# Kernel tuning notes

Measured on AMD Instinct MI355X. Metric: run time of the kernel, lower is better.

The kernel has to match this reference:

```python
import jax, jax.numpy as jnp
import numpy as np

U = 2048
D = 2048
N_HEADS = 16
D_HEAD = D // N_HEADS
FFN_MULT = 4
D_FF = FFN_MULT * D
EPS = 1e-6


def _rmsnorm(x, w):
    # x: [U, D], w: [D]
    ms = jnp.mean(jnp.square(x), axis=-1, keepdims=True)
    return x * jax.lax.rsqrt(ms + EPS) * w


def setup_inputs() -> dict:
    key = jax.random.key(0)
    ks = jax.random.split(key, 12)
    d = {}
    d["x"] = jax.random.normal(ks[0], (U, D), dtype=jnp.float32)
    d["adj_bias"] = jax.random.normal(ks[1], (U, U), dtype=jnp.float32)
    # learned params (torch nn.Linear stores weight as [out, in]; y = x @ W.T)
    init = lambda k, shape, std: jax.random.normal(k, shape, dtype=jnp.float32) * std
    d["norm1_w"] = jnp.ones((D,), dtype=jnp.float32)
    d["norm2_w"] = jnp.ones((D,), dtype=jnp.float32)
    d["wq"] = init(ks[2], (D, D), (1.0 / D) ** 0.5)
    d["wk"] = init(ks[3], (D, D), (1.0 / D) ** 0.5)
    d["wv"] = init(ks[4], (D, D), (1.0 / D) ** 0.5)
    d["wo"] = init(ks[5], (D, D), (2.0 / D) ** 0.5)  # nn.init.normal_ std=(2/D)^0.5
    d["w_up"] = init(ks[6], (D_FF, D), (1.0 / D) ** 0.5)
    d["b_up"] = jnp.zeros((D_FF,), dtype=jnp.float32)
    d["w_down"] = init(ks[7], (D, D_FF), (2.0 / D_FF) ** 0.5)
    d["b_down"] = jnp.zeros((D,), dtype=jnp.float32)
    return d


def reference(x, adj_bias, norm1_w, norm2_w, wq, wk, wv, wo, w_up, b_up, w_down, b_down):
    scale = 1.0 / (D_HEAD ** 0.5)
    h = _rmsnorm(x, norm1_w)
    # project and split heads: [U, D] -> [H, U, d]
    q = (h @ wq.T).reshape(U, N_HEADS, D_HEAD).transpose(1, 0, 2)
    k = (h @ wk.T).reshape(U, N_HEADS, D_HEAD).transpose(1, 0, 2)
    v = (h @ wv.T).reshape(U, N_HEADS, D_HEAD).transpose(1, 0, 2)
    scores = jnp.einsum('hud,hvd->huv', q, k) * scale + adj_bias[None, :, :]
    attn = jax.nn.softmax(scores, axis=-1)
    out = jnp.einsum('huv,hvd->hud', attn, v)  # [H, U, d]
    out = out.transpose(1, 0, 2).reshape(U, D)
    x = x + out @ wo.T
    h2 = _rmsnorm(x, norm2_w)
    ff = jax.nn.gelu(h2 @ w_up.T + b_up, approximate=False)
    x = x + ff @ w_down.T + b_down
    return x
```

## Files before the change

### kernel.cpp

```cpp
#include <hip/hip_runtime.h>
#include <hip/hip_fp16.h>
#include <cstdint>
#include <cstddef>

#define U_DIM 2048
#define D_DIM 2048
#define NH 16
#define DH 128
#define DFF 8192
#define EPS_RMS 1e-6f
#define ATTN_SCALE 0.088388347648318447f

typedef unsigned short u16;
typedef __attribute__((ext_vector_type(4))) float floatx4;
typedef __attribute__((ext_vector_type(8))) short shortx8;

__device__ __forceinline__ float bf2f(u16 u) {
  union { unsigned int i; float f; } v; v.i = ((unsigned int)u) << 16; return v.f;
}
__device__ __forceinline__ u16 f2bf(float f) {
  union { float f; unsigned int i; } v; v.f = f;
  return (u16)((v.i + 0x7fffu + ((v.i >> 16) & 1u)) >> 16);
}
__device__ __forceinline__ u16 f2h(float f) {
  __half h = __float2half_rn(f);
  union { __half h; u16 u; } c; c.h = h; return c.u;
}
__device__ __forceinline__ float h2f(u16 u) {
  union { __half h; u16 u; } c; c.u = u; return __half2float(c.h);
}

__global__ __launch_bounds__(256) void k_f2b(const float* __restrict__ in,
                                             u16* __restrict__ out, int n4) {
  int i = blockIdx.x * 256 + threadIdx.x;
  if (i >= n4) return;
  float4 f = reinterpret_cast<const float4*>(in)[i];
  ushort4 o;
  o.x = f2bf(f.x); o.y = f2bf(f.y); o.z = f2bf(f.z); o.w = f2bf(f.w);
  reinterpret_cast<ushort4*>(out)[i] = o;
}

__global__ __launch_bounds__(256) void k_prep_bias(const float* __restrict__ adj,
                                                   u16* __restrict__ adjp) {
  const int tile = blockIdx.x;
  const int qt = tile >> 4, kt = tile & 15;
  const int t = threadIdx.x;
  const int c16 = t & 15, rblk = t >> 4;
  u16* outt = adjp + (size_t)tile * 16384;
#pragma unroll
  for (int rr = 0; rr < 8; rr++) {
    int r = rblk * 8 + rr;
    const float* src = adj + (size_t)(qt * 128 + r) * U_DIM + kt * 128 + c16;
    ushort4 o0, o1;
    o0.x = f2h(src[0]);    o0.y = f2h(src[16]);  o0.z = f2h(src[32]);  o0.w = f2h(src[48]);
    o1.x = f2h(src[64]);   o1.y = f2h(src[80]);  o1.z = f2h(src[96]);  o1.w = f2h(src[112]);
    ushort4* dst = reinterpret_cast<ushort4*>(outt + ((size_t)c16 * 128 + r) * 8);
    dst[0] = o0; dst[1] = o1;
  }
}

__global__ __launch_bounds__(256) void k_reduce4(
    const u16* __restrict__ p0, const u16* __restrict__ p1,
    const u16* __restrict__ p2, const u16* __restrict__ p3,
    const float* __restrict__ X, const float* __restrict__ bias,
    float* __restrict__ out, int n4) {
  int i = blockIdx.x * 256 + threadIdx.x;
  if (i >= n4) return;
  ushort4 a = reinterpret_cast<const ushort4*>(p0)[i];
  ushort4 b = reinterpret_cast<const ushort4*>(p1)[i];
  ushort4 c = reinterpret_cast<const ushort4*>(p2)[i];
  ushort4 d = reinterpret_cast<const ushort4*>(p3)[i];
  float4 xv = reinterpret_cast<const float4*>(X)[i];
  float4 r;
  r.x = xv.x + bf2f(a.x) + bf2f(b.x) + bf2f(c.x) + bf2f(d.x);
  r.y = xv.y + bf2f(a.y) + bf2f(b.y) + bf2f(c.y) + bf2f(d.y);
  r.z = xv.z + bf2f(a.z) + bf2f(b.z) + bf2f(c.z) + bf2f(d.z);
  r.w = xv.w + bf2f(a.w) + bf2f(b.w) + bf2f(c.w) + bf2f(d.w);
  if (bias) {
    int col = (i * 4) & (D_DIM - 1);
    float4 bv = *reinterpret_cast<const float4*>(bias + col);
    r.x += bv.x; r.y += bv.y; r.z += bv.z; r.w += bv.w;
  }
  reinterpret_cast<float4*>(out)[i] = r;
}

__global__ __launch_bounds__(256) void k_rmsnorm(const float* __restrict__ x,
                                                 const float* __restrict__ w,
                                                 u16* __restrict__ out) {
  const int row = blockIdx.x;
  const int t = threadIdx.x;
  const float4* xr = reinterpret_cast<const float4*>(x + (size_t)row * D_DIM);
  float4 a0 = xr[t], a1 = xr[t + 256];
  float ss = a0.x*a0.x + a0.y*a0.y + a0.z*a0.z + a0.w*a0.w
           + a1.x*a1.x + a1.y*a1.y + a1.z*a1.z + a1.w*a1.w;
#pragma unroll
  for (int off = 32; off > 0; off >>= 1) ss += __shfl_xor(ss, off);
  __shared__ float red[4];
  if ((t & 63) == 0) red[t >> 6] = ss;
  __syncthreads();
  float tot = red[0] + red[1] + red[2] + red[3];
  float r = rsqrtf(tot / (float)D_DIM + EPS_RMS);
  const float4* wr = reinterpret_cast<const float4*>(w);
  float4 w0 = wr[t], w1 = wr[t + 256];
  ushort4 o0, o1;
  o0.x = f2bf(a0.x * r * w0.x); o0.y = f2bf(a0.y * r * w0.y);
  o0.z = f2bf(a0.z * r * w0.z); o0.w = f2bf(a0.w * r * w0.w);
  o1.x = f2bf(a1.x * r * w1.x); o1.y = f2bf(a1.y * r * w1.y);
  o1.z = f2bf(a1.z * r * w1.z); o1.w = f2bf(a1.w * r * w1.w);
  ushort4* op = reinterpret_cast<ushort4*>(out + (size_t)row * D_DIM);
  op[t] = o0; op[t + 256] = o1;
}

__device__ __forceinline__ void async16(u16* lds, const u16* g) {
  __builtin_amdgcn_global_load_lds(
      (__attribute__((address_space(1))) void*)(g),
      (__attribute__((address_space(3))) void*)(lds), 16, 0, 0);
}

#define BK64 64

__device__ __forceinline__ void gemm256_core(
    const u16* __restrict__ A, int lda,
    const u16* __restrict__ B, int ldb,
    int K, int bm, int bn, u16* smem, floatx4 acc[8][4]) {
  const int t = threadIdx.x;
  const int wv = t >> 6, lane = t & 63;
  const int wm = wv >> 2, wn = wv & 3;
  const int fr = lane & 15, kq = lane >> 4;
  const int srow = wv * 8 + (lane >> 3);
  const int scg  = (lane & 7) ^ (lane >> 3);
  const u16* Ag = A + (size_t)(bm + srow) * lda + scg * 8;
  const u16* Bg = B + (size_t)(bn + srow) * ldb + scg * 8;
  u16* AsW = smem + (wv * 8) * 64;
  u16* BsW = smem + 32768 + (wv * 8) * 64;
  const int swz  = fr & 7;
  const int arow = wm * 128 + fr;
  const int brow = wn * 64 + fr;
  const int nt = K / BK64;
#pragma unroll
  for (int r = 0; r < 4; r++) async16(AsW + r * 4096, Ag + (size_t)(r * 64) * lda);
#pragma unroll
  for (int r = 0; r < 4; r++) async16(BsW + r * 4096, Bg + (size_t)(r * 64) * ldb);
  int cur = 0;
  for (int kt = 0; kt < nt; kt++) {
    asm volatile("s_waitcnt vmcnt(0)" ::: "memory");
    __builtin_amdgcn_sched_barrier(0);
    __builtin_amdgcn_s_barrier();
    asm volatile("" ::: "memory");
    if (kt + 1 < nt) {
      const int nb = (cur ^ 1) * 16384;
      const size_t ko = (size_t)(kt + 1) * BK64;
#pragma unroll
      for (int r = 0; r < 4; r++) async16(AsW + nb + r * 4096, Ag + (size_t)(r * 64) * lda + ko);
#pragma unroll
      for (int r = 0; r < 4; r++) async16(BsW + nb + r * 4096, Bg + (size_t)(r * 64) * ldb + ko);
    }
    const u16* Ab = smem + cur * 16384;
    const u16* Bb = smem + 32768 + cur * 16384;
    shortx8 af[4], bf[4];
#pragma unroll
    for (int ph = 0; ph < 4; ph++) {
      const int ksub = ph >> 1;
      const int mh   = ph & 1;
      const int cswz = (((ksub * 4 + kq) ^ swz) * 8);
      if (mh == 0) {
#pragma unroll
        for (int i = 0; i < 4; i++)
          af[i] = *reinterpret_cast<const shortx8*>(Ab + (arow + i * 16) * 64 + cswz);
#pragma unroll
        for (int i = 0; i < 4; i++)
          bf[i] = *reinterpret_cast<const shortx8*>(Bb + (brow + i * 16) * 64 + cswz);
      } else {
#pragma unroll
        for (int i = 0; i < 4; i++)
          af[i] = *reinterpret_cast<const shortx8*>(Ab + (arow + (i + 4) * 16) * 64 + cswz);
      }
      asm volatile("s_waitcnt lgkmcnt(0)" ::: "memory");
      __builtin_amdgcn_sched_barrier(0);
      __builtin_amdgcn_s_setprio(1);
      const int m0 = mh * 4;
#pragma unroll
      for (int i = 0; i < 4; i++)
#pragma unroll
        for (int j = 0; j < 4; j++)
          acc[m0 + i][j] = __builtin_amdgcn_mfma_f32_16x16x32_bf16(af[i], bf[j], acc[m0 + i][j], 0, 0, 0);
      __builtin_amdgcn_s_setprio(0);
      if (ph < 3) { __builtin_amdgcn_s_barrier(); asm volatile("" ::: "memory"); }
    }
    cur ^= 1;
  }
}

#define GEMM256_PRELUDE                                           \
  __shared__ u16 smem[65536];                         \
  floatx4 acc[8][4];                                              \
  {                                                               \
    floatx4 zf = {0.f, 0.f, 0.f, 0.f};                            \
    for (int i = 0; i < 8; i++)                                   \
      for (int j = 0; j < 4; j++) acc[i][j] = zf;                 \
  }                                                               \
  const int bm = blockIdx.y * 256, bn = blockIdx.x * 256;

#define EPILOG256                                                 \
  const int lane_ = threadIdx.x & 63;                             \
  const int wv_ = threadIdx.x >> 6;                               \
  const int fr_ = lane_ & 15, kq_ = lane_ >> 4;                   \
  const int row0 = (wv_ >> 2) * 128 + kq_ * 4;                    \
  const int col0 = (wv_ & 3) * 64 + fr_;

__global__ __launch_bounds__(512, 1) void k_gemm_qkv(
    const u16* __restrict__ A, const u16* __restrict__ B,
    u16* __restrict__ Q, u16* __restrict__ Ko, u16* __restrict__ VT) {
  GEMM256_PRELUDE;
  gemm256_core(A, D_DIM, B, D_DIM, D_DIM, bm, bn, smem, acc);
  EPILOG256;
  if (bn < 4096) {
    u16* C = (bn < 2048) ? Q : Ko;
    const int cb = (bn < 2048) ? bn : bn - 2048;
#pragma unroll
    for (int mt = 0; mt < 8; mt++)
#pragma unroll
      for (int i = 0; i < 4; i++) {
        u16* cr = C + (size_t)(bm + row0 + mt*16 + i) * D_DIM + cb + col0;
#pragma unroll
        for (int nt = 0; nt < 4; nt++) cr[nt*16] = f2bf(acc[mt][nt][i]);
      }
  } else {
    const int cb = bn - 4096;
#pragma unroll
    for (int mt = 0; mt < 8; mt++)
#pragma unroll
      for (int nt = 0; nt < 4; nt++) {
        int col = cb + col0 + nt*16;
        int row = bm + row0 + mt*16;
        ushort4 o;
        o.x = f2bf(acc[mt][nt][0]); o.y = f2bf(acc[mt][nt][1]);
        o.z = f2bf(acc[mt][nt][2]); o.w = f2bf(acc[mt][nt][3]);
        *reinterpret_cast<ushort4*>(VT + (size_t)col * U_DIM + row) = o;
      }
  }
}

__global__ __launch_bounds__(512, 1) void k_gemm_splitk_part(
    const u16* __restrict__ A, int lda, const u16* __restrict__ B, int ldb,
    int Kc, u16* __restrict__ P, size_t pstride, int ldc) {
  GEMM256_PRELUDE;
  const int koff = blockIdx.z * Kc;
  gemm256_core(A + koff, lda, B + koff, ldb, Kc, bm, bn, smem, acc);
  u16* Pz = P + (size_t)blockIdx.z * pstride;
  EPILOG256;
#pragma unroll
  for (int mt = 0; mt < 8; mt++)
#pragma unroll
    for (int i = 0; i < 4; i++) {
      u16* cr = Pz + (size_t)(bm + row0 + mt*16 + i) * ldc + bn + col0;
#pragma unroll
      for (int nt = 0; nt < 4; nt++) cr[nt*16] = f2bf(acc[mt][nt][i]);
    }
}

__device__ __forceinline__ float fast_gelu(float v) {
  float u = v * (0.79788456080286536f + 0.035677408136300125f * v * v);
  float tt = fminf(fmaxf(2.f * u, -40.f), 40.f);
  float e = __expf(tt);
  return 0.5f * v * (1.f + (e - 1.f) / (e + 1.f));
}

__global__ __launch_bounds__(512, 1) void k_gemm_gelu(
    const u16* __restrict__ A, int lda, const u16* __restrict__ B, int ldb,
    int K, const float* __restrict__ bias, u16* __restrict__ C, int ldc) {
  GEMM256_PRELUDE;
  gemm256_core(A, lda, B, ldb, K, bm, bn, smem, acc);
  EPILOG256;
#pragma unroll
  for (int mt = 0; mt < 8; mt++)
#pragma unroll
    for (int i = 0; i < 4; i++) {
      size_t off = (size_t)(bm + row0 + mt*16 + i) * ldc + bn + col0;
#pragma unroll
      for (int nt = 0; nt < 4; nt++) {
        float v = acc[mt][nt][i] + bias[bn + col0 + nt*16];
        C[off + nt*16] = f2bf(fast_gelu(v));
      }
    }
}

__global__ __launch_bounds__(256) void k_flash(
    const u16* __restrict__ Q, const u16* __restrict__ K,
    const u16* __restrict__ VT, const u16* __restrict__ ADJP,
    u16* __restrict__ O) {
  __shared__ u16 smem[18432];
  const int qt = blockIdx.x, gh = blockIdx.y;
  const int t = threadIdx.x, wv = t >> 6, lane = t & 63;
  const int fr = lane & 15, kq = lane >> 4;
  const int c4 = lane & 3, r4 = lane >> 2;

  const u16* gq = Q + (size_t)(qt * 64) * D_DIM + gh * DH;
  const u16* gk = K + gh * DH;
  const u16* gv = VT + (size_t)(gh * DH) * U_DIM;

#pragma unroll
  for (int it = 0; it < 4; it++) {
    int row = wv * 16 + it * 4 + kq;
    int cg = (fr + row) & 15;
    async16(smem + row * 128 + fr * 8, gq + (size_t)row * D_DIM + cg * 8);
  }
  __builtin_amdgcn_s_waitcnt(0);
  __syncthreads();
  shortx8 qf[4];
#pragma unroll
  for (int ks = 0; ks < 4; ks++) {
    int row = wv * 16 + fr;
    int slot = ((ks * 4 + kq) - row) & 15;
    qf[ks] = *reinterpret_cast<const shortx8*>(smem + row * 128 + slot * 8);
  }
  __syncthreads();

  floatx4 oacc[8];
  float lrow[4];
#pragma unroll
  for (int nt = 0; nt < 8; nt++) { floatx4 z = {0.f,0.f,0.f,0.f}; oacc[nt] = z; }
#pragma unroll
  for (int i = 0; i < 4; i++) lrow[i] = 0.f;

  {
    u16* Ks = smem; u16* Vs = smem + 8192;
#pragma unroll
    for (int it = 0; it < 2; it++) {
      int row = wv * 8 + it * 4 + kq;
      int cg = (fr + row) & 15;
      async16(Ks + row * 128 + fr * 8, gk + (size_t)row * D_DIM + cg * 8);
    }
#pragma unroll
    for (int it = 0; it < 2; it++) {
      int row = wv * 32 + it * 16 + r4;
      int cg = (c4 + (row >> 1)) & 3;
      async16(Vs + row * 32 + c4 * 8, gv + (size_t)row * U_DIM + cg * 8);
    }
  }

  u16* Pb = smem + 16384;
  for (int kt = 0; kt < 64; kt++) {
    const int cur = kt & 1;
    u16* Ks = smem + cur * 4096;
    u16* Vs = smem + 8192 + cur * 4096;
    asm volatile("s_waitcnt vmcnt(0)" ::: "memory");
    __builtin_amdgcn_s_barrier();
    asm volatile("" ::: "memory");
    if (kt < 63) {
      u16* Kn = smem + (1 - cur) * 4096;
      u16* Vn = smem + 8192 + (1 - cur) * 4096;
      const u16* gkn = gk + (size_t)((kt + 1) * 32) * D_DIM;
      const u16* gvn = gv + (kt + 1) * 32;
#pragma unroll
      for (int it = 0; it < 2; it++) {
        int row = wv * 8 + it * 4 + kq;
        int cg = (fr + row) & 15;
        async16(Kn + row * 128 + fr * 8, gkn + (size_t)row * D_DIM + cg * 8);
      }
#pragma unroll
      for (int it = 0; it < 2; it++) {
        int row = wv * 32 + it * 16 + r4;
        int cg = (c4 + (row >> 1)) & 3;
        async16(Vn + row * 32 + c4 * 8, gvn + (size_t)row * U_DIM + cg * 8);
      }
    }

    floatx4 sacc[2];
    { floatx4 z = {0.f,0.f,0.f,0.f}; sacc[0] = z; sacc[1] = z; }
#pragma unroll
    for (int ks = 0; ks < 4; ks++) {
      int slot0 = ((ks * 4 + kq) - fr) & 15;
      shortx8 kf0 = *reinterpret_cast<const shortx8*>(Ks + fr * 128 + slot0 * 8);
      int slot1 = ((ks * 4 + kq) - (16 + fr)) & 15;
      shortx8 kf1 = *reinterpret_cast<const shortx8*>(Ks + (16 + fr) * 128 + slot1 * 8);
      sacc[0] = __builtin_amdgcn_mfma_f32_16x16x32_bf16(qf[ks], kf0, sacc[0], 0, 0, 0);
      sacc[1] = __builtin_amdgcn_mfma_f32_16x16x32_bf16(qf[ks], kf1, sacc[1], 0, 0, 0);
    }

    const u16* bt = ADJP + ((size_t)(qt >> 1) * 16 + (kt >> 2)) * 16384 + (kt & 3) * 2;
#pragma unroll
    for (int i = 0; i < 4; i++) {
      int rl = wv * 16 + kq * 4 + i;
      int r128 = (qt & 1) * 64 + rl;
      ushort2 bh = *reinterpret_cast<const ushort2*>(bt + ((size_t)fr * 128 + r128) * 8);
      float s0 = sacc[0][i] * ATTN_SCALE + h2f(bh.x);
      float s1 = sacc[1][i] * ATTN_SCALE + h2f(bh.y);
      float p0 = __expf(fminf(s0, 80.f));
      float p1 = __expf(fminf(s1, 80.f));
      int slot0 = ((fr >> 3) - (rl >> 1)) & 3;
      Pb[rl * 32 + slot0 * 8 + (fr & 7)] = f2bf(p0);
      int slot1 = (((16 + fr) >> 3) - (rl >> 1)) & 3;
      Pb[rl * 32 + slot1 * 8 + (fr & 7)] = f2bf(p1);
      lrow[i] += p0 + p1;
    }
    asm volatile("s_waitcnt lgkmcnt(0)" ::: "memory");
    __builtin_amdgcn_s_barrier();
    asm volatile("" ::: "memory");

    shortx8 pf;
    {
      int row = wv * 16 + fr;
      int slot = (kq - (row >> 1)) & 3;
      pf = *reinterpret_cast<const shortx8*>(Pb + row * 32 + slot * 8);
    }
#pragma unroll
    for (int nt = 0; nt < 8; nt++) {
      int row = nt * 16 + fr;
      int slot = (kq - (row >> 1)) & 3;
      shortx8 vf = *reinterpret_cast<const shortx8*>(Vs + row * 32 + slot * 8);
      oacc[nt] = __builtin_amdgcn_mfma_f32_16x16x32_bf16(pf, vf, oacc[nt], 0, 0, 0);
    }
  }

#pragma unroll
  for (int i = 0; i < 4; i++) {
    int rl = wv * 16 + kq * 4 + i;
    float l = lrow[i];
    l += __shfl_xor(l, 1);
    l += __shfl_xor(l, 2);
    l += __shfl_xor(l, 4);
    l += __shfl_xor(l, 8);
    float inv = 1.f / l;
    u16* orow = O + (size_t)(qt * 64 + rl) * D_DIM + gh * DH + fr;
#pragma unroll
    for (int nt = 0; nt < 8; nt++)
      orow[nt * 16] = f2bf(oacc[nt][i] * inv);
  }
}

extern "C" void kernel_launch(void* const* d_in, const int* in_sizes, int n_in,
                              void* d_out, int out_size, void* d_ws, size_t ws_size,
                              hipStream_t stream) {
  (void)in_sizes; (void)n_in; (void)out_size; (void)ws_size;
  const float* x      = (const float*)d_in[0];
  const float* adj    = (const float*)d_in[1];
  const float* n1w    = (const float*)d_in[2];
  const float* n2w    = (const float*)d_in[3];
  const float* wq     = (const float*)d_in[4];
  const float* wk     = (const float*)d_in[5];
  const float* wv     = (const float*)d_in[6];
  const float* wo     = (const float*)d_in[7];
  const float* w_up   = (const float*)d_in[8];
  const float* b_up   = (const float*)d_in[9];
  const float* w_down = (const float*)d_in[10];
  const float* b_down = (const float*)d_in[11];
  float* out = (float*)d_out;
  char* ws = (char*)d_ws;
  const size_t MB = 1u << 20;
  u16* hb   = (u16*)(ws + 0*MB);
  u16* qb   = (u16*)(ws + 8*MB);
  u16* kb   = (u16*)(ws + 16*MB);
  u16* vtb  = (u16*)(ws + 24*MB);
  u16* adjp = (u16*)(ws + 32*MB);
  u16* aob  = (u16*)(ws + 40*MB);
  u16* wob  = (u16*)(ws + 48*MB);
  u16* wqkv = (u16*)(ws + 56*MB);
  u16* opp  = (u16*)(ws + 8*MB);
  u16* h2b  = (u16*)(ws + 0*MB);
  u16* wub  = (u16*)(ws + 8*MB);
  u16* ffb  = (u16*)(ws + 40*MB);
  u16* wdb  = (u16*)(ws + 72*MB);
  u16* dpp  = (u16*)(ws + 8*MB);

  dim3 blk(256);
  dim3 blk512(512);
  const int n4d = (D_DIM * D_DIM) / 4;
  const int n4f = (DFF * D_DIM) / 4;
  const size_t szd = (size_t)D_DIM * D_DIM;

  k_f2b<<<(n4d + 255) / 256, blk, 0, stream>>>(wq, wqkv, n4d);
  k_f2b<<<(n4d + 255) / 256, blk, 0, stream>>>(wk, wqkv + szd, n4d);
  k_f2b<<<(n4d + 255) / 256, blk, 0, stream>>>(wv, wqkv + 2*szd, n4d);
  k_f2b<<<(n4d + 255) / 256, blk, 0, stream>>>(wo, wob, n4d);
  k_prep_bias<<<256, blk, 0, stream>>>(adj, adjp);
  k_rmsnorm<<<U_DIM, blk, 0, stream>>>(x, n1w, hb);

  k_gemm_qkv<<<dim3(24, 8), blk512, 0, stream>>>(hb, wqkv, qb, kb, vtb);

  k_flash<<<dim3(32, 16), blk, 0, stream>>>(qb, kb, vtb, adjp, aob);

  k_gemm_splitk_part<<<dim3(8, 8, 4), blk512, 0, stream>>>(
      aob, D_DIM, wob, D_DIM, D_DIM/4, opp, szd, D_DIM);
  k_reduce4<<<(n4d + 255) / 256, blk, 0, stream>>>(
      opp, opp + szd, opp + 2*szd, opp + 3*szd, x, nullptr, out, n4d);

  k_rmsnorm<<<U_DIM, blk, 0, stream>>>(out, n2w, h2b);
  k_f2b<<<(n4f + 255) / 256, blk, 0, stream>>>(w_up, wub, n4f);
  k_gemm_gelu<<<dim3(32, 8), blk512, 0, stream>>>(h2b, D_DIM, wub, D_DIM, D_DIM,
                                                  b_up, ffb, DFF);
  k_f2b<<<(n4f + 255) / 256, blk, 0, stream>>>(w_down, wdb, n4f);
  k_gemm_splitk_part<<<dim3(8, 8, 4), blk512, 0, stream>>>(
      ffb, DFF, wdb, DFF, DFF/4, dpp, szd, D_DIM);
  k_reduce4<<<(n4d + 255) / 256, blk, 0, stream>>>(
      dpp, dpp + szd, dpp + 2*szd, dpp + 3*szd, out, b_down, out, n4d);
}
```

Before: 581.9 us.

## Batch weight conversions, fuse residual reduce with RMSNorm, widen flash KV tile

Merges the four D×D weight casts into one launch and the w_up/w_down casts into another. Fuses the split-K partial reduce and residual add with the second RMSNorm, so the residual is not written and then read back by a separate norm kernel. The flash-attention KV tile grows from 32 to 64 keys per iteration, halving loop trips and barriers at the cost of doubling shared memory, which may lower occupancy.

```diff
diff --git a/kernel.cpp b/kernel.cpp
--- a/kernel.cpp
+++ b/kernel.cpp
@@ -30,14 +30,36 @@
   union { __half h; u16 u; } c; c.u = u; return __half2float(c.h);
 }
 
-__global__ __launch_bounds__(256) void k_f2b(const float* __restrict__ in,
-                                             u16* __restrict__ out, int n4) {
-  int i = blockIdx.x * 256 + threadIdx.x;
+__device__ __forceinline__ void f2b_body(const float* __restrict__ in,
+                                         u16* __restrict__ out, int i, int n4) {
   if (i >= n4) return;
   float4 f = reinterpret_cast<const float4*>(in)[i];
   ushort4 o;
   o.x = f2bf(f.x); o.y = f2bf(f.y); o.z = f2bf(f.z); o.w = f2bf(f.w);
   reinterpret_cast<ushort4*>(out)[i] = o;
+}
+
+__global__ __launch_bounds__(256) void k_f2b4(
+    const float* __restrict__ s0, const float* __restrict__ s1,
+    const float* __restrict__ s2, const float* __restrict__ s3,
+    u16* __restrict__ d0, u16* __restrict__ d1,
+    u16* __restrict__ d2, u16* __restrict__ d3, int n4) {
+  const float* s; u16* d;
+  switch (blockIdx.y) {
+    case 0: s = s0; d = d0; break;
+    case 1: s = s1; d = d1; break;
+    case 2: s = s2; d = d2; break;
+    default: s = s3; d = d3; break;
+  }
+  f2b_body(s, d, blockIdx.x * 256 + threadIdx.x, n4);
+}
+
+__global__ __launch_bounds__(256) void k_f2b2(
+    const float* __restrict__ s0, const float* __restrict__ s1,
+    u16* __restrict__ d0, u16* __restrict__ d1, int n4) {
+  const float* s = blockIdx.y ? s1 : s0;
+  u16* d = blockIdx.y ? d1 : d0;
+  f2b_body(s, d, blockIdx.x * 256 + threadIdx.x, n4);
 }
 
 __global__ __launch_bounds__(256) void k_prep_bias(const float* __restrict__ adj,
@@ -84,6 +106,51 @@
   reinterpret_cast<float4*>(out)[i] = r;
 }
 
+__global__ __launch_bounds__(256) void k_reduce4norm(
+    const u16* __restrict__ p0, const u16* __restrict__ p1,
+    const u16* __restrict__ p2, const u16* __restrict__ p3,
+    const float* __restrict__ X, const float* __restrict__ w,
+    float* __restrict__ out, u16* __restrict__ nrm) {
+  const int row = blockIdx.x;
+  const int t = threadIdx.x;
+  const size_t base = (size_t)row * 512;
+  float4 r[2];
+  float ss = 0.f;
+#pragma unroll
+  for (int h = 0; h < 2; h++) {
+    size_t i = base + t + h * 256;
+    ushort4 a = reinterpret_cast<const ushort4*>(p0)[i];
+    ushort4 b = reinterpret_cast<const ushort4*>(p1)[i];
+    ushort4 c = reinterpret_cast<const ushort4*>(p2)[i];
+    ushort4 d = reinterpret_cast<const ushort4*>(p3)[i];
+    float4 xv = reinterpret_cast<const float4*>(X)[i];
+    float4 v;
+    v.x = xv.x + bf2f(a.x) + bf2f(b.x) + bf2f(c.x) + bf2f(d.x);
+    v.y = xv.y + bf2f(a.y) + bf2f(b.y) + bf2f(c.y) + bf2f(d.y);
+    v.z = xv.z + bf2f(a.z) + bf2f(b.z) + bf2f(c.z) + bf2f(d.z);
+    v.w = xv.w + bf2f(a.w) + bf2f(b.w) + bf2f(c.w) + bf2f(d.w);
+    reinterpret_cast<float4*>(out)[i] = v;
+    ss += v.x*v.x + v.y*v.y + v.z*v.z + v.w*v.w;
+    r[h] = v;
+  }
+#pragma unroll
+  for (int off = 32; off > 0; off >>= 1) ss += __shfl_xor(ss, off);
+  __shared__ float red[4];
+  if ((t & 63) == 0) red[t >> 6] = ss;
+  __syncthreads();
+  float tot = red[0] + red[1] + red[2] + red[3];
+  float rms = rsqrtf(tot / (float)D_DIM + EPS_RMS);
+  const float4* wr = reinterpret_cast<const float4*>(w);
+#pragma unroll
+  for (int h = 0; h < 2; h++) {
+    float4 wv = wr[t + h * 256];
+    ushort4 o;
+    o.x = f2bf(r[h].x * rms * wv.x); o.y = f2bf(r[h].y * rms * wv.y);
+    o.z = f2bf(r[h].z * rms * wv.z); o.w = f2bf(r[h].w * rms * wv.w);
+    reinterpret_cast<ushort4*>(nrm)[base + t + h * 256] = o;
+  }
+}
+
 __global__ __launch_bounds__(256) void k_rmsnorm(const float* __restrict__ x,
                                                  const float* __restrict__ w,
                                                  u16* __restrict__ out) {
@@ -289,7 +356,7 @@
     const u16* __restrict__ Q, const u16* __restrict__ K,
     const u16* __restrict__ VT, const u16* __restrict__ ADJP,
     u16* __restrict__ O) {
-  __shared__ u16 smem[18432];
+  __shared__ u16 smem[36864];
   const int qt = blockIdx.x, gh = blockIdx.y;
   const int t = threadIdx.x, wv = t >> 6, lane = t & 63;
   const int fr = lane & 15, kq = lane >> 4;
@@ -324,92 +391,111 @@
   for (int i = 0; i < 4; i++) lrow[i] = 0.f;
 
   {
-    u16* Ks = smem; u16* Vs = smem + 8192;
-#pragma unroll
-    for (int it = 0; it < 2; it++) {
-      int row = wv * 8 + it * 4 + kq;
+    u16* Ks = smem; u16* Vs = smem + 16384;
+#pragma unroll
+    for (int it = 0; it < 4; it++) {
+      int row = wv * 16 + it * 4 + kq;
       int cg = (fr + row) & 15;
       async16(Ks + row * 128 + fr * 8, gk + (size_t)row * D_DIM + cg * 8);
     }
 #pragma unroll
-    for (int it = 0; it < 2; it++) {
-      int row = wv * 32 + it * 16 + r4;
-      int cg = (c4 + (row >> 1)) & 3;
-      async16(Vs + row * 32 + c4 * 8, gv + (size_t)row * U_DIM + cg * 8);
-    }
-  }
-
-  u16* Pb = smem + 16384;
-  for (int kt = 0; kt < 64; kt++) {
-    const int cur = kt & 1;
-    u16* Ks = smem + cur * 4096;
-    u16* Vs = smem + 8192 + cur * 4096;
+    for (int sub = 0; sub < 2; sub++)
+#pragma unroll
+      for (int it = 0; it < 2; it++) {
+        int row = wv * 32 + it * 16 + r4;
+        int cg = (c4 + (row >> 1)) & 3;
+        async16(Vs + sub * 4096 + row * 32 + c4 * 8,
+                gv + (size_t)row * U_DIM + sub * 32 + cg * 8);
+      }
+  }
+
+  u16* Pb = smem + 32768;
+  for (int kt64 = 0; kt64 < 32; kt64++) {
+    const int cur = kt64 & 1;
+    u16* Ks = smem + cur * 8192;
+    u16* Vs = smem + 16384 + cur * 8192;
     asm volatile("s_waitcnt vmcnt(0)" ::: "memory");
     __builtin_amdgcn_s_barrier();
     asm volatile("" ::: "memory");
-    if (kt < 63) {
-      u16* Kn = smem + (1 - cur) * 4096;
-      u16* Vn = smem + 8192 + (1 - cur) * 4096;
-      const u16* gkn = gk + (size_t)((kt + 1) * 32) * D_DIM;
-      const u16* gvn = gv + (kt + 1) * 32;
-#pragma unroll
-      for (int it = 0; it < 2; it++) {
-        int row = wv * 8 + it * 4 + kq;
+    if (kt64 < 31) {
+      u16* Kn = smem + (1 - cur) * 8192;
+      u16* Vn = smem + 16384 + (1 - cur) * 8192;
+      const u16* gkn = gk + (size_t)((kt64 + 1) * 64) * D_DIM;
+      const u16* gvn = gv + (kt64 + 1) * 64;
+#pragma unroll
+      for (int it = 0; it < 4; it++) {
+        int row = wv * 16 + it * 4 + kq;
         int cg = (fr + row) & 15;
         async16(Kn + row * 128 + fr * 8, gkn + (size_t)row * D_DIM + cg * 8);
       }
 #pragma unroll
-      for (int it = 0; it < 2; it++) {
-        int row = wv * 32 + it * 16 + r4;
-        int cg = (c4 + (row >> 1)) & 3;
-        async16(Vn + row * 32 + c4 * 8, gvn + (size_t)row * U_DIM + cg * 8);
-      }
-    }
-
-    floatx4 sacc[2];
-    { floatx4 z = {0.f,0.f,0.f,0.f}; sacc[0] = z; sacc[1] = z; }
+      for (int sub = 0; sub < 2; sub++)
+#pragma unroll
+        for (int it = 0; it < 2; it++) {
+          int row = wv * 32 + it * 16 + r4;
+          int cg = (c4 + (row >> 1)) & 3;
+          async16(Vn + sub * 4096 + row * 32 + c4 * 8,
+                  gvn + (size_t)row * U_DIM + sub * 32 + cg * 8);
+        }
+    }
+
+    floatx4 sacc[4];
+    { floatx4 z = {0.f,0.f,0.f,0.f}; sacc[0]=z; sacc[1]=z; sacc[2]=z; sacc[3]=z; }
 #pragma unroll
     for (int ks = 0; ks < 4; ks++) {
-      int slot0 = ((ks * 4 + kq) - fr) & 15;
-      shortx8 kf0 = *reinterpret_cast<const shortx8*>(Ks + fr * 128 + slot0 * 8);
-      int slot1 = ((ks * 4 + kq) - (16 + fr)) & 15;
-      shortx8 kf1 = *reinterpret_cast<const shortx8*>(Ks + (16 + fr) * 128 + slot1 * 8);
+      int slotA = ((ks * 4 + kq) - fr) & 15;
+      int slotB = ((ks * 4 + kq) - (16 + fr)) & 15;
+      shortx8 kf0 = *reinterpret_cast<const shortx8*>(Ks + fr * 128 + slotA * 8);
+      shortx8 kf1 = *reinterpret_cast<const shortx8*>(Ks + (16 + fr) * 128 + slotB * 8);
+      shortx8 kf2 = *reinterpret_cast<const shortx8*>(Ks + (32 + fr) * 128 + slotA * 8);
+      shortx8 kf3 = *reinterpret_cast<const shortx8*>(Ks + (48 + fr) * 128 + slotB * 8);
       sacc[0] = __builtin_amdgcn_mfma_f32_16x16x32_bf16(qf[ks], kf0, sacc[0], 0, 0, 0);
       sacc[1] = __builtin_amdgcn_mfma_f32_16x16x32_bf16(qf[ks], kf1, sacc[1], 0, 0, 0);
-    }
-
-    const u16* bt = ADJP + ((size_t)(qt >> 1) * 16 + (kt >> 2)) * 16384 + (kt & 3) * 2;
+      sacc[2] = __builtin_amdgcn_mfma_f32_16x16x32_bf16(qf[ks], kf2, sacc[2], 0, 0, 0);
+      sacc[3] = __builtin_amdgcn_mfma_f32_16x16x32_bf16(qf[ks], kf3, sacc[3], 0, 0, 0);
+    }
+
+    const u16* bt = ADJP + ((size_t)(qt >> 1) * 16 + (kt64 >> 1)) * 16384 + (kt64 & 1) * 4;
 #pragma unroll
     for (int i = 0; i < 4; i++) {
       int rl = wv * 16 + kq * 4 + i;
       int r128 = (qt & 1) * 64 + rl;
-      ushort2 bh = *reinterpret_cast<const ushort2*>(bt + ((size_t)fr * 128 + r128) * 8);
+      ushort4 bh = *reinterpret_cast<const ushort4*>(bt + ((size_t)fr * 128 + r128) * 8);
       float s0 = sacc[0][i] * ATTN_SCALE + h2f(bh.x);
       float s1 = sacc[1][i] * ATTN_SCALE + h2f(bh.y);
+      float s2 = sacc[2][i] * ATTN_SCALE + h2f(bh.z);
+      float s3 = sacc[3][i] * ATTN_SCALE + h2f(bh.w);
       float p0 = __expf(fminf(s0, 80.f));
       float p1 = __expf(fminf(s1, 80.f));
+      float p2 = __expf(fminf(s2, 80.f));
+      float p3 = __expf(fminf(s3, 80.f));
       int slot0 = ((fr >> 3) - (rl >> 1)) & 3;
-      Pb[rl * 32 + slot0 * 8 + (fr & 7)] = f2bf(p0);
       int slot1 = (((16 + fr) >> 3) - (rl >> 1)) & 3;
-      Pb[rl * 32 + slot1 * 8 + (fr & 7)] = f2bf(p1);
-      lrow[i] += p0 + p1;
+      Pb[rl * 64 + slot0 * 8 + (fr & 7)] = f2bf(p0);
+      Pb[rl * 64 + slot1 * 8 + (fr & 7)] = f2bf(p1);
+      Pb[rl * 64 + 32 + slot0 * 8 + (fr & 7)] = f2bf(p2);
+      Pb[rl * 64 + 32 + slot1 * 8 + (fr & 7)] = f2bf(p3);
+      lrow[i] += (p0 + p1) + (p2 + p3);
     }
     asm volatile("s_waitcnt lgkmcnt(0)" ::: "memory");
     __builtin_amdgcn_s_barrier();
     asm volatile("" ::: "memory");
 
-    shortx8 pf;
+    shortx8 pf0, pf1;
     {
       int row = wv * 16 + fr;
       int slot = (kq - (row >> 1)) & 3;
-      pf = *reinterpret_cast<const shortx8*>(Pb + row * 32 + slot * 8);
+      pf0 = *reinterpret_cast<const shortx8*>(Pb + row * 64 + slot * 8);
+      pf1 = *reinterpret_cast<const shortx8*>(Pb + row * 64 + 32 + slot * 8);
     }
 #pragma unroll
     for (int nt = 0; nt < 8; nt++) {
       int row = nt * 16 + fr;
       int slot = (kq - (row >> 1)) & 3;
-      shortx8 vf = *reinterpret_cast<const shortx8*>(Vs + row * 32 + slot * 8);
-      oacc[nt] = __builtin_amdgcn_mfma_f32_16x16x32_bf16(pf, vf, oacc[nt], 0, 0, 0);
+      shortx8 vf0 = *reinterpret_cast<const shortx8*>(Vs + row * 32 + slot * 8);
+      shortx8 vf1 = *reinterpret_cast<const shortx8*>(Vs + 4096 + row * 32 + slot * 8);
+      oacc[nt] = __builtin_amdgcn_mfma_f32_16x16x32_bf16(pf0, vf0, oacc[nt], 0, 0, 0);
+      oacc[nt] = __builtin_amdgcn_mfma_f32_16x16x32_bf16(pf1, vf1, oacc[nt], 0, 0, 0);
     }
   }
 
@@ -469,10 +555,8 @@
   const int n4f = (DFF * D_DIM) / 4;
   const size_t szd = (size_t)D_DIM * D_DIM;
 
-  k_f2b<<<(n4d + 255) / 256, blk, 0, stream>>>(wq, wqkv, n4d);
-  k_f2b<<<(n4d + 255) / 256, blk, 0, stream>>>(wk, wqkv + szd, n4d);
-  k_f2b<<<(n4d + 255) / 256, blk, 0, stream>>>(wv, wqkv + 2*szd, n4d);
-  k_f2b<<<(n4d + 255) / 256, blk, 0, stream>>>(wo, wob, n4d);
+  k_f2b4<<<dim3((n4d + 255) / 256, 4), blk, 0, stream>>>(
+      wq, wk, wv, wo, wqkv, wqkv + szd, wqkv + 2*szd, wob, n4d);
   k_prep_bias<<<256, blk, 0, stream>>>(adj, adjp);
   k_rmsnorm<<<U_DIM, blk, 0, stream>>>(x, n1w, hb);
 
@@ -482,14 +566,12 @@
 
   k_gemm_splitk_part<<<dim3(8, 8, 4), blk512, 0, stream>>>(
       aob, D_DIM, wob, D_DIM, D_DIM/4, opp, szd, D_DIM);
-  k_reduce4<<<(n4d + 255) / 256, blk, 0, stream>>>(
-      opp, opp + szd, opp + 2*szd, opp + 3*szd, x, nullptr, out, n4d);
-
-  k_rmsnorm<<<U_DIM, blk, 0, stream>>>(out, n2w, h2b);
-  k_f2b<<<(n4f + 255) / 256, blk, 0, stream>>>(w_up, wub, n4f);
+  k_reduce4norm<<<U_DIM, blk, 0, stream>>>(
+      opp, opp + szd, opp + 2*szd, opp + 3*szd, x, n2w, out, h2b);
+
+  k_f2b2<<<dim3((n4f + 255) / 256, 2), blk, 0, stream>>>(w_up, w_down, wub, wdb, n4f);
   k_gemm_gelu<<<dim3(32, 8), blk512, 0, stream>>>(h2b, D_DIM, wub, D_DIM, D_DIM,
                                                   b_up, ffb, DFF);
-  k_f2b<<<(n4f + 255) / 256, blk, 0, stream>>>(w_down, wdb, n4f);
   k_gemm_splitk_part<<<dim3(8, 8, 4), blk512, 0, stream>>>(
       ffb, DFF, wdb, DFF, DFF/4, dpp, szd, D_DIM);
   k_reduce4<<<(n4d + 255) / 256, blk, 0, stream>>>(
```

After: 542.8 us. 1.07x faster.
